# Optimization experiments

Measured on AMD Instinct MI355X. Metric: run time of the kernel, lower is better.

Reference implementation:

```python
import jax, jax.numpy as jnp
import numpy as np

COMMITMENT_COST = 0.25
NUM_CODEBOOKS = 8192
EMBED_DIM = 256


def setup_inputs() -> dict:
    key = jax.random.key(0)
    kx, kc = jax.random.split(key)
    x = jax.random.normal(kx, (64, 512, 256), dtype=jnp.float32)
    codebook = jax.random.normal(kc, (NUM_CODEBOOKS, EMBED_DIM), dtype=jnp.float32)
    return {"x": x, "codebook": codebook, "hidden_dim": EMBED_DIM}


def reference(x, codebook, hidden_dim):
    # Flatten tokens: [N, D]
    flat = x.reshape(-1, hidden_dim)
    # Squared L2 distances to every codebook entry: [N, K]
    distances = (
        jnp.sum(flat * flat, axis=1, keepdims=True)
        + jnp.sum(codebook * codebook, axis=1)
        - 2.0 * jnp.matmul(flat, codebook.T)
    )
    encoding_indices = jnp.argmin(distances, axis=1)  # [N]
    quantized = jnp.take(codebook, encoding_indices, axis=0).reshape(x.shape)
    # Commitment loss (codebook detached -> plain MSE here in fwd)
    commitment_loss = COMMITMENT_COST * jnp.mean((quantized - x) ** 2)
    # Straight-through estimator
    quantized = x + jax.lax.stop_gradient(quantized - x)
    return quantized, commitment_loss
```

## Files before the change

### kernel.cpp

```cpp
#include <hip/hip_runtime.h>
#include <math.h>

#define N_TOK 32768
#define DDIM  256
#define KCB   8192
#define SLICES 4
#define KS     (KCB / SLICES)
#define TCODES 64
#define NSTEP  (KS / TCODES)
#define MARGIN 1.0f
#define NFBLK  (N_TOK / 4)

typedef _Float16 half_t;
typedef half_t half8 __attribute__((ext_vector_type(8)));
typedef half_t half4 __attribute__((ext_vector_type(4)));
typedef float  f32x4 __attribute__((ext_vector_type(4)));
typedef float  f32x2 __attribute__((ext_vector_type(2)));

#define GLOBAL_AS __attribute__((address_space(1)))
#define LDS_AS    __attribute__((address_space(3)))

__global__ __launch_bounds__(64) void prep_cb(const float* __restrict__ cb,
                                              half_t* __restrict__ cb16,
                                              float* __restrict__ cnorm) {
    int code = blockIdx.x;
    int lane = threadIdx.x;
    f32x4 v = *(const f32x4*)(cb + (size_t)code * DDIM + lane * 4);
    half4 h; h[0]=(half_t)v[0]; h[1]=(half_t)v[1]; h[2]=(half_t)v[2]; h[3]=(half_t)v[3];
    *(half4*)(cb16 + (size_t)code * DDIM + lane * 4) = h;
    float s = v[0]*v[0] + v[1]*v[1] + v[2]*v[2] + v[3]*v[3];
    #pragma unroll
    for (int off = 32; off > 0; off >>= 1) s += __shfl_down(s, off);
    if (lane == 0) cnorm[code] = s;
}

__device__ __forceinline__ half8 ldcvt8(const float* __restrict__ p) {
    f32x4 a = *(const f32x4*)p;
    f32x4 b = *(const f32x4*)(p + 4);
    half8 h;
    h[0]=(half_t)a[0]; h[1]=(half_t)a[1]; h[2]=(half_t)a[2]; h[3]=(half_t)a[3];
    h[4]=(half_t)b[0]; h[5]=(half_t)b[1]; h[6]=(half_t)b[2]; h[7]=(half_t)b[3];
    return h;
}

__device__ __forceinline__ float packkey(float a, unsigned code) {
    return __uint_as_float((__float_as_uint(a) & 0xFFFFE000u) | code);
}

__global__ __launch_bounds__(256, 2)
void passA(const float* __restrict__ x, const half_t* __restrict__ cb16,
           const float* __restrict__ cnorm, float* __restrict__ cand) {

    __shared__ __align__(16) half_t buf[2][TCODES * 256];

    const int tid  = threadIdx.x;
    const int w    = tid >> 6;
    const int lane = tid & 63;
    const int quad = lane >> 4;
    const int mcol = lane & 15;
    const int tokBase   = blockIdx.x * 256 + w * 64;
    const int codeBase0 = blockIdx.y * KS;

    half8 afrag[4][8];
    #pragma unroll
    for (int rt = 0; rt < 4; rt++) {
        const float* xr = x + (size_t)(tokBase + rt * 16 + mcol) * DDIM + quad * 8;
        #pragma unroll
        for (int dk = 0; dk < 8; dk++)
            afrag[rt][dk] = ldcvt8(xr + dk * 32);
    }

    int boff[8];
    #pragma unroll
    for (int dk = 0; dk < 8; dk++)
        boff[dk] = mcol * 256 + (((dk * 4 + quad) ^ (mcol & 7)) * 8);

    float k0[4][4], k1[4][4];
    #pragma unroll
    for (int rt = 0; rt < 4; rt++)
        #pragma unroll
        for (int r = 0; r < 4; r++) { k0[rt][r] = -INFINITY; k1[rt][r] = -INFINITY; }

    const char* cbbase = (const char*)(cb16 + (size_t)codeBase0 * DDIM);
    #define STAGE(nt, b)                                                        \
        {                                                                       \
            const char* srcb = cbbase + (size_t)(nt) * (TCODES * 512);          \
            _Pragma("unroll")                                                   \
            for (int o = 0; o < 8; o++) {                                       \
                int L = o * 256 + tid;                                          \
                int r = L >> 5, c = (L & 31) ^ (r & 7);                         \
                __builtin_amdgcn_global_load_lds(                               \
                    (const GLOBAL_AS void*)(srcb + r * 512 + c * 16),           \
                    (LDS_AS void*)&buf[b][(o * 256 + w * 64) * 8], 16, 0, 0);   \
            }                                                                   \
        }

    STAGE(0, 0)
    __syncthreads();

    for (int nt = 0; nt < NSTEP; nt++) {
        if (nt + 1 < NSTEP) STAGE(nt + 1, (nt + 1) & 1)

        const half_t* cur = buf[nt & 1];
        const int codeBase = codeBase0 + nt * TCODES;

        #pragma unroll
        for (int p = 0; p < 2; p++) {
            const float mc0 = -0.5f * cnorm[codeBase + p * 32 + mcol];
            const float mc1 = -0.5f * cnorm[codeBase + p * 32 + 16 + mcol];
            f32x4 acc[2][4];
            #pragma unroll
            for (int rt = 0; rt < 4; rt++) {
                acc[0][rt][0]=mc0; acc[0][rt][1]=mc0; acc[0][rt][2]=mc0; acc[0][rt][3]=mc0;
                acc[1][rt][0]=mc1; acc[1][rt][1]=mc1; acc[1][rt][2]=mc1; acc[1][rt][3]=mc1;
            }
            const half_t* crow0 = cur + (p * 32) * 256;
            const half_t* crow1 = cur + (p * 32 + 16) * 256;
            #pragma unroll
            for (int dk = 0; dk < 8; dk++) {
                half8 bf0 = *(const half8*)(crow0 + boff[dk]);
                half8 bf1 = *(const half8*)(crow1 + boff[dk]);
                #pragma unroll
                for (int rt = 0; rt < 4; rt++) {
                    acc[0][rt] = __builtin_amdgcn_mfma_f32_16x16x32_f16(afrag[rt][dk], bf0, acc[0][rt], 0, 0, 0);
                    acc[1][rt] = __builtin_amdgcn_mfma_f32_16x16x32_f16(afrag[rt][dk], bf1, acc[1][rt], 0, 0, 0);
                }
            }
            const unsigned code0 = (unsigned)(codeBase + p * 32 + mcol);
            const unsigned code1 = code0 + 16;
            #pragma unroll
            for (int rt = 0; rt < 4; rt++)
                #pragma unroll
                for (int r = 0; r < 4; r++) {
                    float a = packkey(acc[0][rt][r], code0);
                    float b = packkey(acc[1][rt][r], code1);
                    k1[rt][r] = fmaxf(k1[rt][r], __builtin_amdgcn_fmed3f(k0[rt][r], a, b));
                    k0[rt][r] = fmaxf(fmaxf(k0[rt][r], a), b);
                }
        }
        __syncthreads();
    }

    #pragma unroll
    for (int s = 1; s < 16; s <<= 1) {
        #pragma unroll
        for (int rt = 0; rt < 4; rt++)
            #pragma unroll
            for (int r = 0; r < 4; r++) {
                float o0 = __shfl_xor(k0[rt][r], s, 64);
                float o1 = __shfl_xor(k1[rt][r], s, 64);
                float n1 = fmaxf(fminf(k0[rt][r], o0), fmaxf(k1[rt][r], o1));
                k0[rt][r] = fmaxf(k0[rt][r], o0);
                k1[rt][r] = n1;
            }
    }
    if (mcol == 0) {
        #pragma unroll
        for (int rt = 0; rt < 4; rt++)
            #pragma unroll
            for (int r = 0; r < 4; r++) {
                int token = tokBase + rt * 16 + quad * 4 + r;
                f32x2 kk; kk[0] = k0[rt][r]; kk[1] = k1[rt][r];
                *(f32x2*)&cand[(size_t)token * (SLICES * 2) + blockIdx.y * 2] = kk;
            }
    }
}

__global__ __launch_bounds__(256) void finalize_kernel(
    const float* __restrict__ x, const float* __restrict__ cb,
    const float* __restrict__ cnorm, const float* __restrict__ cand,
    float* __restrict__ out, float* __restrict__ partials) {

    const int tid = threadIdx.x, w = tid >> 6, lane = tid & 63;
    const int token = blockIdx.x * 4 + w;
    const float* xrow = x + (size_t)token * DDIM;

    f32x4 ka = *(const f32x4*)(cand + (size_t)token * 8);
    f32x4 kb = *(const f32x4*)(cand + (size_t)token * 8 + 4);
    float v[8] = {ka[0], ka[1], ka[2], ka[3], kb[0], kb[1], kb[2], kb[3]};
    float t0 = -INFINITY, t1 = -INFINITY;
    #pragma unroll
    for (int j = 0; j < 8; j++) {
        float m = fminf(t0, v[j]);
        t0 = fmaxf(t0, v[j]);
        t1 = fmaxf(t1, m);
    }
    int bidx = (int)(__float_as_uint(t0) & 0x1FFFu);

    if (!(t0 - t1 > MARGIN)) {
        const int j = lane >> 3, sub = lane & 7;
        int cj = (int)(__float_as_uint(v[j]) & 0x1FFFu);
        const float* crow = cb + (size_t)cj * DDIM;
        float p = 0.0f;
        #pragma unroll
        for (int c = 0; c < 8; c++) {
            f32x4 xa = *(const f32x4*)(xrow + c * 32 + sub * 4);
            f32x4 ca = *(const f32x4*)(crow + c * 32 + sub * 4);
            p += xa[0]*ca[0] + xa[1]*ca[1] + xa[2]*ca[2] + xa[3]*ca[3];
        }
        p += __shfl_xor(p, 1, 64);
        p += __shfl_xor(p, 2, 64);
        p += __shfl_xor(p, 4, 64);
        float bd = cnorm[cj] - 2.0f * p;
        int   bi = cj;
        #pragma unroll
        for (int s = 8; s < 64; s <<= 1) {
            float od = __shfl_xor(bd, s, 64);
            int   oi = __shfl_xor(bi, s, 64);
            if (od < bd || (od == bd && oi < bi)) { bd = od; bi = oi; }
        }
        bidx = bi;
    }

    f32x4 cv = *(const f32x4*)(cb + (size_t)bidx * DDIM + lane * 4);
    f32x4 xv = *(const f32x4*)(xrow + lane * 4);
    *(f32x4*)(out + (size_t)token * DDIM + lane * 4) = cv;
    float d0 = cv[0]-xv[0], d1 = cv[1]-xv[1], d2 = cv[2]-xv[2], d3 = cv[3]-xv[3];
    float lsum = d0*d0 + d1*d1 + d2*d2 + d3*d3;

    __shared__ float red[256];
    red[tid] = lsum;
    __syncthreads();
    #pragma unroll
    for (int s = 128; s > 0; s >>= 1) {
        if (tid < s) red[tid] += red[tid + s];
        __syncthreads();
    }
    if (tid == 0) partials[blockIdx.x] = red[0];
}

__global__ __launch_bounds__(256) void reduce_loss(const float* __restrict__ partials,
                                                   float* __restrict__ out) {
    const int tid = threadIdx.x;
    float s = 0.0f;
    #pragma unroll
    for (int i = 0; i < 8; i++) {
        f32x4 v = *(const f32x4*)(partials + (size_t)(i * 256 + tid) * 4);
        s += v[0] + v[1] + v[2] + v[3];
    }
    __shared__ float red[256];
    red[tid] = s;
    __syncthreads();
    #pragma unroll
    for (int st = 128; st > 0; st >>= 1) {
        if (tid < st) red[tid] += red[tid + st];
        __syncthreads();
    }
    if (tid == 0)
        out[(size_t)N_TOK * DDIM] = red[0] * (0.25f / (float)((size_t)N_TOK * DDIM));
}

extern "C" void kernel_launch(void* const* d_in, const int* in_sizes, int n_in,
                              void* d_out, int out_size, void* d_ws, size_t ws_size,
                              hipStream_t stream) {
    const float* x  = (const float*)d_in[0];
    const float* cb = (const float*)d_in[1];
    float* out = (float*)d_out;

    half_t* cb16     = (half_t*)d_ws;
    float*  cnorm    = (float*)(cb16 + (size_t)KCB * DDIM);
    float*  cand     = cnorm + KCB;
    float*  partials = cand + (size_t)N_TOK * 8;

    prep_cb<<<KCB, 64, 0, stream>>>(cb, cb16, cnorm);
    dim3 gA(N_TOK / 256, SLICES);
    passA<<<gA, 256, 0, stream>>>(x, cb16, cnorm, cand);
    finalize_kernel<<<NFBLK, 256, 0, stream>>>(x, cb, cnorm, cand, out, partials);
    reduce_loss<<<1, 256, 0, stream>>>(partials, out);
}
```

Measured before the change: 226.6 us.

## Shrink passA blocks and code tiles, fold loss reduction into finalize

The distance kernel now uses 128-thread blocks covering 128 tokens and stages 32 codes per step instead of 64. This halves the LDS per block, allows more resident blocks and doubles the grid, at the cost of twice as many barrier steps over the codebook. The separate single-block loss-reduction kernel is removed. Instead, finalize uses an atomic counter, reset in prep_cb, so the last block to finish sums the partials, saving one launch.

```diff
diff --git a/kernel.cpp b/kernel.cpp
--- a/kernel.cpp
+++ b/kernel.cpp
@@ -6,7 +6,7 @@
 #define KCB   8192
 #define SLICES 4
 #define KS     (KCB / SLICES)
-#define TCODES 64
+#define TCODES 32
 #define NSTEP  (KS / TCODES)
 #define MARGIN 1.0f
 #define NFBLK  (N_TOK / 4)
@@ -22,7 +22,8 @@
 
 __global__ __launch_bounds__(64) void prep_cb(const float* __restrict__ cb,
                                               half_t* __restrict__ cb16,
-                                              float* __restrict__ cnorm) {
+                                              float* __restrict__ cnorm,
+                                              int* __restrict__ counter) {
     int code = blockIdx.x;
     int lane = threadIdx.x;
     f32x4 v = *(const f32x4*)(cb + (size_t)code * DDIM + lane * 4);
@@ -32,6 +33,7 @@
     #pragma unroll
     for (int off = 32; off > 0; off >>= 1) s += __shfl_down(s, off);
     if (lane == 0) cnorm[code] = s;
+    if (code == 0 && lane == 0) *counter = 0;
 }
 
 __device__ __forceinline__ half8 ldcvt8(const float* __restrict__ p) {
@@ -47,7 +49,7 @@
     return __uint_as_float((__float_as_uint(a) & 0xFFFFE000u) | code);
 }
 
-__global__ __launch_bounds__(256, 2)
+__global__ __launch_bounds__(128, 2)
 void passA(const float* __restrict__ x, const half_t* __restrict__ cb16,
            const float* __restrict__ cnorm, float* __restrict__ cand) {
 
@@ -58,7 +60,7 @@
     const int lane = tid & 63;
     const int quad = lane >> 4;
     const int mcol = lane & 15;
-    const int tokBase   = blockIdx.x * 256 + w * 64;
+    const int tokBase   = blockIdx.x * 128 + w * 64;
     const int codeBase0 = blockIdx.y * KS;
 
     half8 afrag[4][8];
@@ -87,11 +89,11 @@
             const char* srcb = cbbase + (size_t)(nt) * (TCODES * 512);          \
             _Pragma("unroll")                                                   \
             for (int o = 0; o < 8; o++) {                                       \
-                int L = o * 256 + tid;                                          \
+                int L = o * 128 + tid;                                          \
                 int r = L >> 5, c = (L & 31) ^ (r & 7);                         \
                 __builtin_amdgcn_global_load_lds(                               \
                     (const GLOBAL_AS void*)(srcb + r * 512 + c * 16),           \
-                    (LDS_AS void*)&buf[b][(o * 256 + w * 64) * 8], 16, 0, 0);   \
+                    (LDS_AS void*)&buf[b][(o * 128 + w * 64) * 8], 16, 0, 0);   \
             }                                                                   \
         }
 
@@ -104,40 +106,37 @@
         const half_t* cur = buf[nt & 1];
         const int codeBase = codeBase0 + nt * TCODES;
 
-        #pragma unroll
-        for (int p = 0; p < 2; p++) {
-            const float mc0 = -0.5f * cnorm[codeBase + p * 32 + mcol];
-            const float mc1 = -0.5f * cnorm[codeBase + p * 32 + 16 + mcol];
-            f32x4 acc[2][4];
+        const float mc0 = -0.5f * cnorm[codeBase + mcol];
+        const float mc1 = -0.5f * cnorm[codeBase + 16 + mcol];
+        f32x4 acc[2][4];
+        #pragma unroll
+        for (int rt = 0; rt < 4; rt++) {
+            acc[0][rt][0]=mc0; acc[0][rt][1]=mc0; acc[0][rt][2]=mc0; acc[0][rt][3]=mc0;
+            acc[1][rt][0]=mc1; acc[1][rt][1]=mc1; acc[1][rt][2]=mc1; acc[1][rt][3]=mc1;
+        }
+        const half_t* crow0 = cur;
+        const half_t* crow1 = cur + 16 * 256;
+        #pragma unroll
+        for (int dk = 0; dk < 8; dk++) {
+            half8 bf0 = *(const half8*)(crow0 + boff[dk]);
+            half8 bf1 = *(const half8*)(crow1 + boff[dk]);
             #pragma unroll
             for (int rt = 0; rt < 4; rt++) {
-                acc[0][rt][0]=mc0; acc[0][rt][1]=mc0; acc[0][rt][2]=mc0; acc[0][rt][3]=mc0;
-                acc[1][rt][0]=mc1; acc[1][rt][1]=mc1; acc[1][rt][2]=mc1; acc[1][rt][3]=mc1;
-            }
-            const half_t* crow0 = cur + (p * 32) * 256;
-            const half_t* crow1 = cur + (p * 32 + 16) * 256;
-            #pragma unroll
-            for (int dk = 0; dk < 8; dk++) {
-                half8 bf0 = *(const half8*)(crow0 + boff[dk]);
-                half8 bf1 = *(const half8*)(crow1 + boff[dk]);
-                #pragma unroll
-                for (int rt = 0; rt < 4; rt++) {
-                    acc[0][rt] = __builtin_amdgcn_mfma_f32_16x16x32_f16(afrag[rt][dk], bf0, acc[0][rt], 0, 0, 0);
-                    acc[1][rt] = __builtin_amdgcn_mfma_f32_16x16x32_f16(afrag[rt][dk], bf1, acc[1][rt], 0, 0, 0);
-                }
-            }
-            const unsigned code0 = (unsigned)(codeBase + p * 32 + mcol);
-            const unsigned code1 = code0 + 16;
-            #pragma unroll
-            for (int rt = 0; rt < 4; rt++)
-                #pragma unroll
-                for (int r = 0; r < 4; r++) {
-                    float a = packkey(acc[0][rt][r], code0);
-                    float b = packkey(acc[1][rt][r], code1);
-                    k1[rt][r] = fmaxf(k1[rt][r], __builtin_amdgcn_fmed3f(k0[rt][r], a, b));
-                    k0[rt][r] = fmaxf(fmaxf(k0[rt][r], a), b);
-                }
-        }
+                acc[0][rt] = __builtin_amdgcn_mfma_f32_16x16x32_f16(afrag[rt][dk], bf0, acc[0][rt], 0, 0, 0);
+                acc[1][rt] = __builtin_amdgcn_mfma_f32_16x16x32_f16(afrag[rt][dk], bf1, acc[1][rt], 0, 0, 0);
+            }
+        }
+        const unsigned code0 = (unsigned)(codeBase + mcol);
+        const unsigned code1 = code0 + 16;
+        #pragma unroll
+        for (int rt = 0; rt < 4; rt++)
+            #pragma unroll
+            for (int r = 0; r < 4; r++) {
+                float a = packkey(acc[0][rt][r], code0);
+                float b = packkey(acc[1][rt][r], code1);
+                k1[rt][r] = fmaxf(k1[rt][r], __builtin_amdgcn_fmed3f(k0[rt][r], a, b));
+                k0[rt][r] = fmaxf(fmaxf(k0[rt][r], a), b);
+            }
         __syncthreads();
     }
 
@@ -169,7 +168,8 @@
 __global__ __launch_bounds__(256) void finalize_kernel(
     const float* __restrict__ x, const float* __restrict__ cb,
     const float* __restrict__ cnorm, const float* __restrict__ cand,
-    float* __restrict__ out, float* __restrict__ partials) {
+    float* __restrict__ out, float* __restrict__ partials,
+    int* __restrict__ counter) {
 
     const int tid = threadIdx.x, w = tid >> 6, lane = tid & 63;
     const int token = blockIdx.x * 4 + w;
@@ -219,6 +219,7 @@
     float lsum = d0*d0 + d1*d1 + d2*d2 + d3*d3;
 
     __shared__ float red[256];
+    __shared__ int isLast;
     red[tid] = lsum;
     __syncthreads();
     #pragma unroll
@@ -226,28 +227,26 @@
         if (tid < s) red[tid] += red[tid + s];
         __syncthreads();
     }
-    if (tid == 0) partials[blockIdx.x] = red[0];
-}
-
-__global__ __launch_bounds__(256) void reduce_loss(const float* __restrict__ partials,
-                                                   float* __restrict__ out) {
-    const int tid = threadIdx.x;
-    float s = 0.0f;
-    #pragma unroll
-    for (int i = 0; i < 8; i++) {
-        f32x4 v = *(const f32x4*)(partials + (size_t)(i * 256 + tid) * 4);
-        s += v[0] + v[1] + v[2] + v[3];
-    }
-    __shared__ float red[256];
-    red[tid] = s;
+    if (tid == 0) {
+        partials[blockIdx.x] = red[0];
+        __threadfence();
+        isLast = (atomicAdd(counter, 1) == NFBLK - 1);
+    }
     __syncthreads();
-    #pragma unroll
-    for (int st = 128; st > 0; st >>= 1) {
-        if (tid < st) red[tid] += red[tid + st];
+    if (isLast) {
+        __threadfence();
+        float s = 0.0f;
+        for (int i = tid; i < NFBLK; i += 256) s += partials[i];
+        red[tid] = s;
         __syncthreads();
-    }
-    if (tid == 0)
-        out[(size_t)N_TOK * DDIM] = red[0] * (0.25f / (float)((size_t)N_TOK * DDIM));
+        #pragma unroll
+        for (int st = 128; st > 0; st >>= 1) {
+            if (tid < st) red[tid] += red[tid + st];
+            __syncthreads();
+        }
+        if (tid == 0)
+            out[(size_t)N_TOK * DDIM] = red[0] * (0.25f / (float)((size_t)N_TOK * DDIM));
+    }
 }
 
 extern "C" void kernel_launch(void* const* d_in, const int* in_sizes, int n_in,
@@ -261,10 +260,10 @@
     float*  cnorm    = (float*)(cb16 + (size_t)KCB * DDIM);
     float*  cand     = cnorm + KCB;
     float*  partials = cand + (size_t)N_TOK * 8;
-
-    prep_cb<<<KCB, 64, 0, stream>>>(cb, cb16, cnorm);
-    dim3 gA(N_TOK / 256, SLICES);
-    passA<<<gA, 256, 0, stream>>>(x, cb16, cnorm, cand);
-    finalize_kernel<<<NFBLK, 256, 0, stream>>>(x, cb, cnorm, cand, out, partials);
-    reduce_loss<<<1, 256, 0, stream>>>(partials, out);
-}
+    int*    counter  = (int*)(partials + NFBLK);
+
+    prep_cb<<<KCB, 64, 0, stream>>>(cb, cb16, cnorm, counter);
+    dim3 gA(N_TOK / 128, SLICES);
+    passA<<<gA, 128, 0, stream>>>(x, cb16, cnorm, cand);
+    finalize_kernel<<<NFBLK, 256, 0, stream>>>(x, cb, cnorm, cand, out, partials, counter);
+}
```

Result: slower. 485.8 us (+114.3%).

## Drop LDS staging in distance GEMM, read codebook fragments directly from global

Applied to the files above, without the earlier changes.

The main distance kernel no longer double-buffers codebook tiles into shared memory with async global-to-LDS loads and barriers. Each lane now loads its B fragments straight from global memory (relying on L2/L1 reuse across the block's four waves) and the per-tile syncthreads are removed. Separately, the refinement pass skips the exact fp32 dot product for candidates whose approximate score is already more than the margin below the best. This trades LDS traffic and barrier stalls for redundant global/cache loads per wave and exposed load latency.

```diff
diff --git a/kernel.cpp b/kernel.cpp
--- a/kernel.cpp
+++ b/kernel.cpp
@@ -6,8 +6,6 @@
 #define KCB   8192
 #define SLICES 4
 #define KS     (KCB / SLICES)
-#define TCODES 64
-#define NSTEP  (KS / TCODES)
 #define MARGIN 1.0f
 #define NFBLK  (N_TOK / 4)
 
@@ -16,9 +14,6 @@
 typedef half_t half4 __attribute__((ext_vector_type(4)));
 typedef float  f32x4 __attribute__((ext_vector_type(4)));
 typedef float  f32x2 __attribute__((ext_vector_type(2)));
-
-#define GLOBAL_AS __attribute__((address_space(1)))
-#define LDS_AS    __attribute__((address_space(3)))
 
 __global__ __launch_bounds__(64) void prep_cb(const float* __restrict__ cb,
                                               half_t* __restrict__ cb16,
@@ -51,8 +46,6 @@
 void passA(const float* __restrict__ x, const half_t* __restrict__ cb16,
            const float* __restrict__ cnorm, float* __restrict__ cand) {
 
-    __shared__ __align__(16) half_t buf[2][TCODES * 256];
-
     const int tid  = threadIdx.x;
     const int w    = tid >> 6;
     const int lane = tid & 63;
@@ -70,75 +63,48 @@
             afrag[rt][dk] = ldcvt8(xr + dk * 32);
     }
 
-    int boff[8];
-    #pragma unroll
-    for (int dk = 0; dk < 8; dk++)
-        boff[dk] = mcol * 256 + (((dk * 4 + quad) ^ (mcol & 7)) * 8);
-
     float k0[4][4], k1[4][4];
     #pragma unroll
     for (int rt = 0; rt < 4; rt++)
         #pragma unroll
         for (int r = 0; r < 4; r++) { k0[rt][r] = -INFINITY; k1[rt][r] = -INFINITY; }
 
-    const char* cbbase = (const char*)(cb16 + (size_t)codeBase0 * DDIM);
-    #define STAGE(nt, b)                                                        \
-        {                                                                       \
-            const char* srcb = cbbase + (size_t)(nt) * (TCODES * 512);          \
-            _Pragma("unroll")                                                   \
-            for (int o = 0; o < 8; o++) {                                       \
-                int L = o * 256 + tid;                                          \
-                int r = L >> 5, c = (L & 31) ^ (r & 7);                         \
-                __builtin_amdgcn_global_load_lds(                               \
-                    (const GLOBAL_AS void*)(srcb + r * 512 + c * 16),           \
-                    (LDS_AS void*)&buf[b][(o * 256 + w * 64) * 8], 16, 0, 0);   \
-            }                                                                   \
-        }
-
-    STAGE(0, 0)
-    __syncthreads();
-
-    for (int nt = 0; nt < NSTEP; nt++) {
-        if (nt + 1 < NSTEP) STAGE(nt + 1, (nt + 1) & 1)
-
-        const half_t* cur = buf[nt & 1];
-        const int codeBase = codeBase0 + nt * TCODES;
-
-        #pragma unroll
-        for (int p = 0; p < 2; p++) {
-            const float mc0 = -0.5f * cnorm[codeBase + p * 32 + mcol];
-            const float mc1 = -0.5f * cnorm[codeBase + p * 32 + 16 + mcol];
-            f32x4 acc[2][4];
+    const half_t* brow = cb16 + (size_t)(codeBase0 + mcol) * DDIM + quad * 8;
+    const float*  cnp  = cnorm + codeBase0 + mcol;
+
+    for (int ct = 0; ct < KS / 32; ct++) {
+        const half_t* r0 = brow + (size_t)ct * 32 * DDIM;
+        const half_t* r1 = r0 + 16 * DDIM;
+        const float mc0 = -0.5f * cnp[ct * 32];
+        const float mc1 = -0.5f * cnp[ct * 32 + 16];
+
+        f32x4 acc[2][4];
+        #pragma unroll
+        for (int rt = 0; rt < 4; rt++) {
+            acc[0][rt][0]=mc0; acc[0][rt][1]=mc0; acc[0][rt][2]=mc0; acc[0][rt][3]=mc0;
+            acc[1][rt][0]=mc1; acc[1][rt][1]=mc1; acc[1][rt][2]=mc1; acc[1][rt][3]=mc1;
+        }
+        #pragma unroll
+        for (int dk = 0; dk < 8; dk++) {
+            half8 bf0 = *(const half8*)(r0 + dk * 32);
+            half8 bf1 = *(const half8*)(r1 + dk * 32);
             #pragma unroll
             for (int rt = 0; rt < 4; rt++) {
-                acc[0][rt][0]=mc0; acc[0][rt][1]=mc0; acc[0][rt][2]=mc0; acc[0][rt][3]=mc0;
-                acc[1][rt][0]=mc1; acc[1][rt][1]=mc1; acc[1][rt][2]=mc1; acc[1][rt][3]=mc1;
-            }
-            const half_t* crow0 = cur + (p * 32) * 256;
-            const half_t* crow1 = cur + (p * 32 + 16) * 256;
-            #pragma unroll
-            for (int dk = 0; dk < 8; dk++) {
-                half8 bf0 = *(const half8*)(crow0 + boff[dk]);
-                half8 bf1 = *(const half8*)(crow1 + boff[dk]);
-                #pragma unroll
-                for (int rt = 0; rt < 4; rt++) {
-                    acc[0][rt] = __builtin_amdgcn_mfma_f32_16x16x32_f16(afrag[rt][dk], bf0, acc[0][rt], 0, 0, 0);
-                    acc[1][rt] = __builtin_amdgcn_mfma_f32_16x16x32_f16(afrag[rt][dk], bf1, acc[1][rt], 0, 0, 0);
-                }
-            }
-            const unsigned code0 = (unsigned)(codeBase + p * 32 + mcol);
-            const unsigned code1 = code0 + 16;
-            #pragma unroll
-            for (int rt = 0; rt < 4; rt++)
-                #pragma unroll
-                for (int r = 0; r < 4; r++) {
-                    float a = packkey(acc[0][rt][r], code0);
-                    float b = packkey(acc[1][rt][r], code1);
-                    k1[rt][r] = fmaxf(k1[rt][r], __builtin_amdgcn_fmed3f(k0[rt][r], a, b));
-                    k0[rt][r] = fmaxf(fmaxf(k0[rt][r], a), b);
-                }
-        }
-        __syncthreads();
+                acc[0][rt] = __builtin_amdgcn_mfma_f32_16x16x32_f16(afrag[rt][dk], bf0, acc[0][rt], 0, 0, 0);
+                acc[1][rt] = __builtin_amdgcn_mfma_f32_16x16x32_f16(afrag[rt][dk], bf1, acc[1][rt], 0, 0, 0);
+            }
+        }
+        const unsigned code0 = (unsigned)(codeBase0 + ct * 32 + mcol);
+        const unsigned code1 = code0 + 16;
+        #pragma unroll
+        for (int rt = 0; rt < 4; rt++)
+            #pragma unroll
+            for (int r = 0; r < 4; r++) {
+                float a = packkey(acc[0][rt][r], code0);
+                float b = packkey(acc[1][rt][r], code1);
+                k1[rt][r] = fmaxf(k1[rt][r], __builtin_amdgcn_fmed3f(k0[rt][r], a, b));
+                k0[rt][r] = fmaxf(fmaxf(k0[rt][r], a), b);
+            }
     }
 
     #pragma unroll
@@ -189,19 +155,22 @@
 
     if (!(t0 - t1 > MARGIN)) {
         const int j = lane >> 3, sub = lane & 7;
-        int cj = (int)(__float_as_uint(v[j]) & 0x1FFFu);
-        const float* crow = cb + (size_t)cj * DDIM;
+        int  cj   = (int)(__float_as_uint(v[j]) & 0x1FFFu);
+        bool live = (v[j] >= t0 - MARGIN);
         float p = 0.0f;
-        #pragma unroll
-        for (int c = 0; c < 8; c++) {
-            f32x4 xa = *(const f32x4*)(xrow + c * 32 + sub * 4);
-            f32x4 ca = *(const f32x4*)(crow + c * 32 + sub * 4);
-            p += xa[0]*ca[0] + xa[1]*ca[1] + xa[2]*ca[2] + xa[3]*ca[3];
+        if (live) {
+            const float* crow = cb + (size_t)cj * DDIM;
+            #pragma unroll
+            for (int c = 0; c < 8; c++) {
+                f32x4 xa = *(const f32x4*)(xrow + c * 32 + sub * 4);
+                f32x4 ca = *(const f32x4*)(crow + c * 32 + sub * 4);
+                p += xa[0]*ca[0] + xa[1]*ca[1] + xa[2]*ca[2] + xa[3]*ca[3];
+            }
         }
         p += __shfl_xor(p, 1, 64);
         p += __shfl_xor(p, 2, 64);
         p += __shfl_xor(p, 4, 64);
-        float bd = cnorm[cj] - 2.0f * p;
+        float bd = live ? (cnorm[cj] - 2.0f * p) : INFINITY;
         int   bi = cj;
         #pragma unroll
         for (int s = 8; s < 64; s <<= 1) {
```

After: 352.1 us. +55.4%, slower.

## Register-staged codebook prefetch with smaller tiles and skip dead refine candidates

Applied to the files above, without the earlier changes.

Staging of codebook tiles now goes through register prefetch (global load into registers two steps ahead, then an LDS store after compute) instead of direct global-to-LDS loads. The tile is halved to 32 codes per step, so each buffer and the LDS footprint shrink while the number of barriers per slice doubles. The fp32 refine pass now skips the dot product for candidates whose key is more than the margin below the best, which saves loads and FLOPs in the fallback path. The register prefetch adds VGPR pressure, and the extra syncs may reduce overlap.

```diff
diff --git a/kernel.cpp b/kernel.cpp
--- a/kernel.cpp
+++ b/kernel.cpp
@@ -6,7 +6,7 @@
 #define KCB   8192
 #define SLICES 4
 #define KS     (KCB / SLICES)
-#define TCODES 64
+#define TCODES 32
 #define NSTEP  (KS / TCODES)
 #define MARGIN 1.0f
 #define NFBLK  (N_TOK / 4)
@@ -16,9 +16,6 @@
 typedef half_t half4 __attribute__((ext_vector_type(4)));
 typedef float  f32x4 __attribute__((ext_vector_type(4)));
 typedef float  f32x2 __attribute__((ext_vector_type(2)));
-
-#define GLOBAL_AS __attribute__((address_space(1)))
-#define LDS_AS    __attribute__((address_space(3)))
 
 __global__ __launch_bounds__(64) void prep_cb(const float* __restrict__ cb,
                                               half_t* __restrict__ cb16,
@@ -82,63 +79,71 @@
         for (int r = 0; r < 4; r++) { k0[rt][r] = -INFINITY; k1[rt][r] = -INFINITY; }
 
     const char* cbbase = (const char*)(cb16 + (size_t)codeBase0 * DDIM);
-    #define STAGE(nt, b)                                                        \
+    int goff[4];
+    #pragma unroll
+    for (int o = 0; o < 4; o++) {
+        int L = o * 256 + tid, r = L >> 5, c = (L & 31) ^ (r & 7);
+        goff[o] = r * 512 + c * 16;
+    }
+    half8 pf[4];
+    #define LOAD(nt)                                                            \
         {                                                                       \
             const char* srcb = cbbase + (size_t)(nt) * (TCODES * 512);          \
             _Pragma("unroll")                                                   \
-            for (int o = 0; o < 8; o++) {                                       \
-                int L = o * 256 + tid;                                          \
-                int r = L >> 5, c = (L & 31) ^ (r & 7);                         \
-                __builtin_amdgcn_global_load_lds(                               \
-                    (const GLOBAL_AS void*)(srcb + r * 512 + c * 16),           \
-                    (LDS_AS void*)&buf[b][(o * 256 + w * 64) * 8], 16, 0, 0);   \
-            }                                                                   \
-        }
-
-    STAGE(0, 0)
+            for (int o = 0; o < 4; o++)                                         \
+                pf[o] = *(const half8*)(srcb + goff[o]);                        \
+        }
+    #define COMMIT(b)                                                           \
+        {                                                                       \
+            _Pragma("unroll")                                                   \
+            for (int o = 0; o < 4; o++)                                         \
+                *(half8*)&buf[b][(o * 256 + tid) * 8] = pf[o];                  \
+        }
+
+    LOAD(0)
+    COMMIT(0)
     __syncthreads();
+    LOAD(1)
 
     for (int nt = 0; nt < NSTEP; nt++) {
-        if (nt + 1 < NSTEP) STAGE(nt + 1, (nt + 1) & 1)
-
         const half_t* cur = buf[nt & 1];
         const int codeBase = codeBase0 + nt * TCODES;
-
-        #pragma unroll
-        for (int p = 0; p < 2; p++) {
-            const float mc0 = -0.5f * cnorm[codeBase + p * 32 + mcol];
-            const float mc1 = -0.5f * cnorm[codeBase + p * 32 + 16 + mcol];
-            f32x4 acc[2][4];
+        const float mc0 = -0.5f * cnorm[codeBase + mcol];
+        const float mc1 = -0.5f * cnorm[codeBase + 16 + mcol];
+
+        f32x4 acc[2][4];
+        #pragma unroll
+        for (int rt = 0; rt < 4; rt++) {
+            acc[0][rt][0]=mc0; acc[0][rt][1]=mc0; acc[0][rt][2]=mc0; acc[0][rt][3]=mc0;
+            acc[1][rt][0]=mc1; acc[1][rt][1]=mc1; acc[1][rt][2]=mc1; acc[1][rt][3]=mc1;
+        }
+        const half_t* crow0 = cur;
+        const half_t* crow1 = cur + 16 * 256;
+        #pragma unroll
+        for (int dk = 0; dk < 8; dk++) {
+            half8 bf0 = *(const half8*)(crow0 + boff[dk]);
+            half8 bf1 = *(const half8*)(crow1 + boff[dk]);
             #pragma unroll
             for (int rt = 0; rt < 4; rt++) {
-                acc[0][rt][0]=mc0; acc[0][rt][1]=mc0; acc[0][rt][2]=mc0; acc[0][rt][3]=mc0;
-                acc[1][rt][0]=mc1; acc[1][rt][1]=mc1; acc[1][rt][2]=mc1; acc[1][rt][3]=mc1;
-            }
-            const half_t* crow0 = cur + (p * 32) * 256;
-            const half_t* crow1 = cur + (p * 32 + 16) * 256;
-            #pragma unroll
-            for (int dk = 0; dk < 8; dk++) {
-                half8 bf0 = *(const half8*)(crow0 + boff[dk]);
-                half8 bf1 = *(const half8*)(crow1 + boff[dk]);
-                #pragma unroll
-                for (int rt = 0; rt < 4; rt++) {
-                    acc[0][rt] = __builtin_amdgcn_mfma_f32_16x16x32_f16(afrag[rt][dk], bf0, acc[0][rt], 0, 0, 0);
-                    acc[1][rt] = __builtin_amdgcn_mfma_f32_16x16x32_f16(afrag[rt][dk], bf1, acc[1][rt], 0, 0, 0);
-                }
-            }
-            const unsigned code0 = (unsigned)(codeBase + p * 32 + mcol);
-            const unsigned code1 = code0 + 16;
-            #pragma unroll
-            for (int rt = 0; rt < 4; rt++)
-                #pragma unroll
-                for (int r = 0; r < 4; r++) {
-                    float a = packkey(acc[0][rt][r], code0);
-                    float b = packkey(acc[1][rt][r], code1);
-                    k1[rt][r] = fmaxf(k1[rt][r], __builtin_amdgcn_fmed3f(k0[rt][r], a, b));
-                    k0[rt][r] = fmaxf(fmaxf(k0[rt][r], a), b);
-                }
-        }
+                acc[0][rt] = __builtin_amdgcn_mfma_f32_16x16x32_f16(afrag[rt][dk], bf0, acc[0][rt], 0, 0, 0);
+                acc[1][rt] = __builtin_amdgcn_mfma_f32_16x16x32_f16(afrag[rt][dk], bf1, acc[1][rt], 0, 0, 0);
+            }
+        }
+        const unsigned code0 = (unsigned)(codeBase + mcol);
+        const unsigned code1 = code0 + 16;
+        #pragma unroll
+        for (int rt = 0; rt < 4; rt++)
+            #pragma unroll
+            for (int r = 0; r < 4; r++) {
+                float a = packkey(acc[0][rt][r], code0);
+                float b = packkey(acc[1][rt][r], code1);
+                k1[rt][r] = fmaxf(k1[rt][r], __builtin_amdgcn_fmed3f(k0[rt][r], a, b));
+                k0[rt][r] = fmaxf(fmaxf(k0[rt][r], a), b);
+            }
+
+        if (nt + 1 < NSTEP) COMMIT((nt + 1) & 1)
         __syncthreads();
+        if (nt + 2 < NSTEP) LOAD(nt + 2)
     }
 
     #pragma unroll
@@ -189,19 +194,22 @@
 
     if (!(t0 - t1 > MARGIN)) {
         const int j = lane >> 3, sub = lane & 7;
-        int cj = (int)(__float_as_uint(v[j]) & 0x1FFFu);
-        const float* crow = cb + (size_t)cj * DDIM;
+        int  cj   = (int)(__float_as_uint(v[j]) & 0x1FFFu);
+        bool live = (v[j] >= t0 - MARGIN);
         float p = 0.0f;
-        #pragma unroll
-        for (int c = 0; c < 8; c++) {
-            f32x4 xa = *(const f32x4*)(xrow + c * 32 + sub * 4);
-            f32x4 ca = *(const f32x4*)(crow + c * 32 + sub * 4);
-            p += xa[0]*ca[0] + xa[1]*ca[1] + xa[2]*ca[2] + xa[3]*ca[3];
+        if (live) {
+            const float* crow = cb + (size_t)cj * DDIM;
+            #pragma unroll
+            for (int c = 0; c < 8; c++) {
+                f32x4 xa = *(const f32x4*)(xrow + c * 32 + sub * 4);
+                f32x4 ca = *(const f32x4*)(crow + c * 32 + sub * 4);
+                p += xa[0]*ca[0] + xa[1]*ca[1] + xa[2]*ca[2] + xa[3]*ca[3];
+            }
         }
         p += __shfl_xor(p, 1, 64);
         p += __shfl_xor(p, 2, 64);
         p += __shfl_xor(p, 4, 64);
-        float bd = cnorm[cj] - 2.0f * p;
+        float bd = live ? (cnorm[cj] - 2.0f * p) : INFINITY;
         int   bi = cj;
         #pragma unroll
         for (int s = 8; s < 64; s <<= 1) {
```

Result: no change. 228.8 us (+0.9%).
